# Kernel optimization log

Measured on AMD Instinct MI355X. Metric: run time of the kernel, lower is better.

Reference implementation:

```python
import jax, jax.numpy as jnp
import numpy as np

B, L, C, H = 8, 16384, 128, 4
EPS = 1e-5


def setup_inputs() -> dict:
    key = jax.random.key(0)
    k1, k2, k3, k4 = jax.random.split(key, 4)
    return {
        "x": jax.random.normal(k1, (B, L, C), dtype=jnp.float32),
        "W_qkv": jax.random.normal(k2, (3 * C, C), dtype=jnp.float32) * (C ** -0.5),
        "W_out": jax.random.normal(k3, (C, C), dtype=jnp.float32) * (C ** -0.5),
        "b_out": jax.random.normal(k4, (C,), dtype=jnp.float32) * 0.01,
        "gn_w": jnp.ones((C,), dtype=jnp.float32),
        "gn_b": jnp.zeros((C,), dtype=jnp.float32),
    }


def reference(x, W_qkv, W_out, b_out, gn_w, gn_b):
    b, l, c = x.shape
    h = H
    d = c // h                      # dim_head
    scale = d ** -0.5
    xc = jnp.swapaxes(x, 1, 2)      # [b, c, l]
    # 1x1 conv == channel matmul
    qkv = jnp.einsum('oc,bcl->bol', W_qkv, xc)     # [b, 3c, l]
    q, k, v = jnp.split(qkv, 3, axis=1)
    q = q.reshape(b, h, d, l)
    k = k.reshape(b, h, d, l)
    v = v.reshape(b, h, d, l)
    q = jax.nn.softmax(q, axis=2) * scale          # softmax over head-dim
    k = jax.nn.softmax(k, axis=3)                  # softmax over length
    context = jnp.einsum('bhcj,bhdj->bhcd', k, v)  # [b, h, d, d]
    out = jnp.einsum('bhcd,bhdi->bhci', context, q)  # [b, h, d, l]
    out = out.reshape(b, h * d, l)
    out = jnp.einsum('oc,bcl->bol', W_out, out) + b_out[None, :, None]
    # GroupNorm(1, c): normalize over (channel, length) per sample
    mean = jnp.mean(out, axis=(1, 2), keepdims=True)
    var = jnp.var(out, axis=(1, 2), keepdims=True)
    out = (out - mean) * jax.lax.rsqrt(var + EPS)
    out = out * gn_w[None, :, None] + gn_b[None, :, None]
    return jnp.swapaxes(out, 1, 2)                 # [b, l, c]
```

## Files before the change

### kernel.cpp

```cpp
#include <hip/hip_runtime.h>

#define BATCH 8
#define SEQL 16384
#define NCH 128
#define NH 4
#define HD 32
#define GEPS 1e-5f

typedef __bf16 bf16x8 __attribute__((ext_vector_type(8)));
typedef __bf16 bf16x4 __attribute__((ext_vector_type(4)));
typedef float f32x4 __attribute__((ext_vector_type(4)));

#define WKV_B   0
#define WQ_B    65536
#define WO_B    98304
#define CTXB_B  131072
#define GNS_B   196608
#define CTXP_B  262144


__global__ void k_prep(const float* __restrict__ wqkv, const float* __restrict__ wout,
                       char* __restrict__ wsb) {
    int i = blockIdx.x * 256 + threadIdx.x;
    __bf16* wkvb = (__bf16*)(wsb + WKV_B);
    __bf16* wqb  = (__bf16*)(wsb + WQ_B);
    __bf16* wob  = (__bf16*)(wsb + WO_B);
    if (i < 384 * 128) {
        int o = i >> 7, c = i & 127;
        __bf16 v = (__bf16)wqkv[i];
        if (o < 128) wqb[o * 128 + c] = v;
        else         wkvb[(o - 128) * 128 + c] = v;
    }
    if (i < 128 * 128) wob[i] = (__bf16)wout[i];
    if (i < 16) ((float*)(wsb + GNS_B))[i] = 0.f;
}

__global__ __launch_bounds__(256, 3) void k_pass1(const float* __restrict__ x,
                                                  char* __restrict__ wsb, int P) {
    __shared__ __attribute__((aligned(16))) __bf16 xb[8352];
    __shared__ __attribute__((aligned(16))) __bf16 ekv[16464];
    const int t = threadIdx.x;
    const int lane = t & 63, wave = t >> 6;
    const int n16 = lane & 15, q = lane >> 4;
    const int batch = blockIdx.x / P, sub = blockIdx.x % P;
    const int nrep = 256 / P;
    const __bf16* __restrict__ wkvb = (const __bf16*)(wsb + WKV_B);

    bf16x8 aw[4][4];
#pragma unroll
    for (int mt = 0; mt < 4; mt++)
#pragma unroll
        for (int ks = 0; ks < 4; ks++)
            aw[mt][ks] = *(const bf16x8*)&wkvb[(wave * 64 + mt * 16 + n16) * 128 + ks * 32 + q * 8];

    f32x4 ctxacc[2][2];
#pragma unroll
    for (int i = 0; i < 2; i++)
#pragma unroll
        for (int j = 0; j < 2; j++) ctxacc[i][j] = (f32x4){0.f, 0.f, 0.f, 0.f};
    float zacc[4][4];
#pragma unroll
    for (int i = 0; i < 4; i++)
#pragma unroll
        for (int j = 0; j < 4; j++) zacc[i][j] = 0.f;

    for (int rep = 0; rep < nrep; rep++) {
        const int chunk = sub + rep * P;
        const float* xg = x + (size_t)(batch * SEQL + chunk * 64) * NCH;
#pragma unroll
        for (int r = 0; r < 8; r++) {
            int e = t + r * 256;
            int tok = e >> 5, c4 = (e & 31) * 4;
            float4 v = ((const float4*)xg)[e];
            bf16x4 h; h.x = (__bf16)v.x; h.y = (__bf16)v.y; h.z = (__bf16)v.z; h.w = (__bf16)v.w;
            *(bf16x4*)&xb[(c4 >> 5) * 2088 + ((c4 >> 3) & 3) * 520 + tok * 8 + (c4 & 7)] = h;
        }
        __syncthreads();

#pragma unroll
        for (int half = 0; half < 2; half++) {
            f32x4 kvacc[4][2];
#pragma unroll
            for (int i = 0; i < 4; i++)
#pragma unroll
                for (int j = 0; j < 2; j++) kvacc[i][j] = (f32x4){0.f, 0.f, 0.f, 0.f};
#pragma unroll
            for (int ks = 0; ks < 4; ks++) {
                bf16x8 b[2];
#pragma unroll
                for (int nl = 0; nl < 2; nl++)
                    b[nl] = *(const bf16x8*)&xb[ks * 2088 + q * 520 + ((half * 2 + nl) * 16 + n16) * 8];
#pragma unroll
                for (int mt = 0; mt < 4; mt++)
#pragma unroll
                    for (int nl = 0; nl < 2; nl++)
                        kvacc[mt][nl] = __builtin_amdgcn_mfma_f32_16x16x32_bf16(
                            aw[mt][ks], b[nl], kvacc[mt][nl], 0, 0, 0);
            }
#pragma unroll
            for (int mt = 0; mt < 4; mt++)
#pragma unroll
                for (int nl = 0; nl < 2; nl++) {
                    int tt = (half * 2 + nl) * 16 + n16;
                    int base = (tt >> 5) * 8232 + ((tt >> 3) & 3) * 2056 + (tt & 7);
#pragma unroll
                    for (int r = 0; r < 4; r++) {
                        float vv = kvacc[mt][nl][r];
                        if (wave < 2) { vv = __expf(vv); zacc[mt][r] += vv; }
                        int o = wave * 64 + mt * 16 + q * 4 + r;
                        ekv[base + o * 8] = (__bf16)vv;
                    }
                }
        }
        __syncthreads();

#pragma unroll
        for (int ks2 = 0; ks2 < 2; ks2++) {
            bf16x8 ea[2], vb[2];
#pragma unroll
            for (int ml = 0; ml < 2; ml++) {
                ea[ml] = *(const bf16x8*)&ekv[ks2 * 8232 + q * 2056 + (wave * 32 + ml * 16 + n16) * 8];
                vb[ml] = *(const bf16x8*)&ekv[ks2 * 8232 + q * 2056 + (128 + wave * 32 + ml * 16 + n16) * 8];
            }
#pragma unroll
            for (int ml = 0; ml < 2; ml++)
#pragma unroll
                for (int nl = 0; nl < 2; nl++)
                    ctxacc[ml][nl] = __builtin_amdgcn_mfma_f32_16x16x32_bf16(
                        ea[ml], vb[nl], ctxacc[ml][nl], 0, 0, 0);
        }
        __syncthreads();
    }

    float* ctxp = (float*)(wsb + CTXP_B) + (size_t)blockIdx.x * 4096 + wave * 1024;
#pragma unroll
    for (int ml = 0; ml < 2; ml++)
#pragma unroll
        for (int nl = 0; nl < 2; nl++)
#pragma unroll
            for (int r = 0; r < 4; r++)
                ctxp[(ml * 16 + q * 4 + r) * 32 + nl * 16 + n16] = ctxacc[ml][nl][r];
    if (wave < 2) {
        float* zpT = (float*)(wsb + CTXP_B) + (size_t)BATCH * P * 4096;
#pragma unroll
        for (int mt = 0; mt < 4; mt++)
#pragma unroll
            for (int r = 0; r < 4; r++) {
                float z = zacc[mt][r];
                z += __shfl_xor(z, 1); z += __shfl_xor(z, 2);
                z += __shfl_xor(z, 4); z += __shfl_xor(z, 8);
                if (n16 == 0)
                    zpT[((size_t)batch * 128 + wave * 64 + mt * 16 + q * 4 + r) * P + sub] = z;
            }
    }
}

__global__ __launch_bounds__(256) void k_reduce(char* __restrict__ wsb, int P) {
    __shared__ float red[4][64];
    __shared__ float zw[4];
    const int tid = threadIdx.x;
    const int b = blockIdx.x >> 6, eg = blockIdx.x & 63;
    const int elemBase = eg * 64;
    const float* ctxp = (const float*)(wsb + CTXP_B);
    const float* zpT = ctxp + (size_t)BATCH * P * 4096;

    {
        int hc2 = tid >> 7, pslot = tid & 127;
        float zs = 0.f;
        for (int p = pslot; p < P; p += 128)
            zs += zpT[((size_t)b * 128 + eg * 2 + hc2) * P + p];
#pragma unroll
        for (int off = 32; off > 0; off >>= 1) zs += __shfl_xor(zs, off);
        if ((tid & 63) == 0) zw[tid >> 6] = zs;
    }
    {
        int pg = tid >> 6, e = tid & 63;
        int cnt = P >> 2;
        const float* base = ctxp + ((size_t)(b * P + pg * cnt)) * 4096 + elemBase + e;
        float cs = 0.f;
        for (int k = 0; k < cnt; k++) cs += base[(size_t)k * 4096];
        red[pg][e] = cs;
    }
    __syncthreads();
    if (tid < 64) {
        float tot = red[0][tid] + red[1][tid] + red[2][tid] + red[3][tid];
        float zs = zw[(tid >> 5) * 2] + zw[(tid >> 5) * 2 + 1];
        ((__bf16*)(wsb + CTXB_B))[(size_t)b * 4096 + elemBase + tid] = (__bf16)(tot / zs);
    }
}

__global__ __launch_bounds__(256, 4) void k_pass2(const float* __restrict__ x,
                                                  const float* __restrict__ bout,
                                                  char* __restrict__ wsb,
                                                  float* __restrict__ out) {
    __shared__ __attribute__((aligned(16))) __bf16 xb[8352];
    __shared__ __attribute__((aligned(16))) __bf16 pB[8352];
    __shared__ float gred[8];
    const int t = threadIdx.x;
    const int lane = t & 63, wave = t >> 6;
    const int n16 = lane & 15, q = lane >> 4;
    const int batch = blockIdx.x >> 8, chunk = blockIdx.x & 255;
    const __bf16* __restrict__ wqb = (const __bf16*)(wsb + WQ_B);
    const __bf16* __restrict__ wob = (const __bf16*)(wsb + WO_B);
    const __bf16* __restrict__ ctxb = (const __bf16*)(wsb + CTXB_B);

    const size_t tok0 = (size_t)batch * SEQL + chunk * 64;
    const float* xg = x + tok0 * NCH;
#pragma unroll
    for (int r = 0; r < 8; r++) {
        int e = t + r * 256;
        int tok = e >> 5, c4 = (e & 31) * 4;
        float4 v = ((const float4*)xg)[e];
        bf16x4 h; h.x = (__bf16)v.x; h.y = (__bf16)v.y; h.z = (__bf16)v.z; h.w = (__bf16)v.w;
        *(bf16x4*)&xb[(c4 >> 5) * 2088 + ((c4 >> 3) & 3) * 520 + tok * 8 + (c4 & 7)] = h;
    }
    __syncthreads();

    f32x4 qacc[2][4];
#pragma unroll
    for (int i = 0; i < 2; i++)
#pragma unroll
        for (int j = 0; j < 4; j++) qacc[i][j] = (f32x4){0.f, 0.f, 0.f, 0.f};
#pragma unroll
    for (int ks = 0; ks < 4; ks++) {
        bf16x8 aq_k[2];
#pragma unroll
        for (int ml = 0; ml < 2; ml++)
            aq_k[ml] = *(const bf16x8*)&wqb[(wave * 32 + ml * 16 + n16) * 128 + ks * 32 + q * 8];
        bf16x8 b[4];
#pragma unroll
        for (int nt = 0; nt < 4; nt++)
            b[nt] = *(const bf16x8*)&xb[ks * 2088 + q * 520 + (nt * 16 + n16) * 8];
#pragma unroll
        for (int ml = 0; ml < 2; ml++)
#pragma unroll
            for (int nt = 0; nt < 4; nt++)
                qacc[ml][nt] = __builtin_amdgcn_mfma_f32_16x16x32_bf16(
                    aq_k[ml], b[nt], qacc[ml][nt], 0, 0, 0);
    }
#pragma unroll
    for (int nt = 0; nt < 4; nt++) {
        float ss = 0.f;
#pragma unroll
        for (int ml = 0; ml < 2; ml++)
#pragma unroll
            for (int r = 0; r < 4; r++) {
                float e = __expf(qacc[ml][nt][r]);
                qacc[ml][nt][r] = e;
                ss += e;
            }
        ss += __shfl_xor(ss, 16);
        ss += __shfl_xor(ss, 32);
        float inv = 0.17677669529663687f / ss;
#pragma unroll
        for (int ml = 0; ml < 2; ml++)
#pragma unroll
            for (int r = 0; r < 4; r++) qacc[ml][nt][r] *= inv;
    }
#pragma unroll
    for (int ml = 0; ml < 2; ml++)
#pragma unroll
        for (int nt = 0; nt < 4; nt++) {
            bf16x4 h;
            h.x = (__bf16)qacc[ml][nt][0]; h.y = (__bf16)qacc[ml][nt][1];
            h.z = (__bf16)qacc[ml][nt][2]; h.w = (__bf16)qacc[ml][nt][3];
            *(bf16x4*)&pB[wave * 2088 + (ml * 2 + (q >> 1)) * 520 +
                          (nt * 16 + n16) * 8 + (q & 1) * 4] = h;
        }
    __syncthreads();
    bf16x8 actx[2];
#pragma unroll
    for (int ml = 0; ml < 2; ml++)
        actx[ml] = *(const bf16x8*)&ctxb[((size_t)(batch * 4 + wave) * 32 + ml * 16 + n16) * 32 + q * 8];
    f32x4 aacc[2][4];
#pragma unroll
    for (int ml = 0; ml < 2; ml++)
#pragma unroll
        for (int nt = 0; nt < 4; nt++) {
            bf16x8 pb = *(const bf16x8*)&pB[wave * 2088 + q * 520 + (nt * 16 + n16) * 8];
            aacc[ml][nt] = __builtin_amdgcn_mfma_f32_16x16x32_bf16(
                actx[ml], pb, (f32x4){0.f, 0.f, 0.f, 0.f}, 0, 0, 0);
        }
    __bf16* attB = xb;
#pragma unroll
    for (int ml = 0; ml < 2; ml++)
#pragma unroll
        for (int nt = 0; nt < 4; nt++) {
            bf16x4 h;
            h.x = (__bf16)aacc[ml][nt][0]; h.y = (__bf16)aacc[ml][nt][1];
            h.z = (__bf16)aacc[ml][nt][2]; h.w = (__bf16)aacc[ml][nt][3];
            *(bf16x4*)&attB[wave * 2088 + (ml * 2 + (q >> 1)) * 520 +
                            (nt * 16 + n16) * 8 + (q & 1) * 4] = h;
        }
    __syncthreads();
    f32x4 oacc[2][4];
#pragma unroll
    for (int i = 0; i < 2; i++)
#pragma unroll
        for (int j = 0; j < 4; j++) oacc[i][j] = (f32x4){0.f, 0.f, 0.f, 0.f};
#pragma unroll
    for (int ks = 0; ks < 4; ks++) {
        bf16x8 ao_k[2];
#pragma unroll
        for (int ml = 0; ml < 2; ml++)
            ao_k[ml] = *(const bf16x8*)&wob[(wave * 32 + ml * 16 + n16) * 128 + ks * 32 + q * 8];
        bf16x8 b[4];
#pragma unroll
        for (int nt = 0; nt < 4; nt++)
            b[nt] = *(const bf16x8*)&attB[ks * 2088 + q * 520 + (nt * 16 + n16) * 8];
#pragma unroll
        for (int ml = 0; ml < 2; ml++)
#pragma unroll
            for (int nt = 0; nt < 4; nt++)
                oacc[ml][nt] = __builtin_amdgcn_mfma_f32_16x16x32_bf16(
                    ao_k[ml], b[nt], oacc[ml][nt], 0, 0, 0);
    }
    float4 bias[2];
#pragma unroll
    for (int ml = 0; ml < 2; ml++)
        bias[ml] = *(const float4*)&bout[wave * 32 + ml * 16 + q * 4];
    float s1 = 0.f, s2 = 0.f;
#pragma unroll
    for (int ml = 0; ml < 2; ml++)
#pragma unroll
        for (int nt = 0; nt < 4; nt++) {
            float4 vv;
            vv.x = oacc[ml][nt][0] + bias[ml].x;
            vv.y = oacc[ml][nt][1] + bias[ml].y;
            vv.z = oacc[ml][nt][2] + bias[ml].z;
            vv.w = oacc[ml][nt][3] + bias[ml].w;
            s1 += vv.x + vv.y + vv.z + vv.w;
            s2 += vv.x * vv.x + vv.y * vv.y + vv.z * vv.z + vv.w * vv.w;
            *(float4*)&out[(tok0 + nt * 16 + n16) * NCH + wave * 32 + ml * 16 + q * 4] = vv;
        }
#pragma unroll
    for (int off = 32; off > 0; off >>= 1) {
        s1 += __shfl_xor(s1, off);
        s2 += __shfl_xor(s2, off);
    }
    if (lane == 0) { gred[wave * 2 + 0] = s1; gred[wave * 2 + 1] = s2; }
    __syncthreads();
    if (t < 2) {
        float s = gred[t] + gred[2 + t] + gred[4 + t] + gred[6 + t];
        atomicAdd(&((float*)(wsb + GNS_B))[batch * 2 + t], s);
    }
}

__global__ __launch_bounds__(256) void k_gnorm(float* __restrict__ out,
                                               const char* __restrict__ wsb,
                                               const float* __restrict__ gw,
                                               const float* __restrict__ gb) {
    size_t base4 = ((size_t)blockIdx.x * 256 + threadIdx.x) * 2;
    int b = (int)(base4 >> 19);
    const float* gns = (const float*)(wsb + GNS_B);
    const float n = (float)NCH * (float)SEQL;
    float mean = gns[b * 2] / n;
    float var = gns[b * 2 + 1] / n - mean * mean;
    float rstd = rsqrtf(var + GEPS);
    int cbase = (int)((base4 & 31) * 4);
    float4 w0 = *(const float4*)&gw[cbase];
    float4 w1 = *(const float4*)&gw[cbase + 4];
    float4 b0 = *(const float4*)&gb[cbase];
    float4 b1 = *(const float4*)&gb[cbase + 4];
    float4 v0 = ((float4*)out)[base4];
    float4 v1 = ((float4*)out)[base4 + 1];
    v0.x = (v0.x - mean) * rstd * w0.x + b0.x;
    v0.y = (v0.y - mean) * rstd * w0.y + b0.y;
    v0.z = (v0.z - mean) * rstd * w0.z + b0.z;
    v0.w = (v0.w - mean) * rstd * w0.w + b0.w;
    v1.x = (v1.x - mean) * rstd * w1.x + b1.x;
    v1.y = (v1.y - mean) * rstd * w1.y + b1.y;
    v1.z = (v1.z - mean) * rstd * w1.z + b1.z;
    v1.w = (v1.w - mean) * rstd * w1.w + b1.w;
    ((float4*)out)[base4] = v0;
    ((float4*)out)[base4 + 1] = v1;
}

extern "C" void kernel_launch(void* const* d_in, const int* in_sizes, int n_in,
                              void* d_out, int out_size, void* d_ws, size_t ws_size,
                              hipStream_t stream) {
    const float* x    = (const float*)d_in[0];
    const float* wqkv = (const float*)d_in[1];
    const float* wout = (const float*)d_in[2];
    const float* bout = (const float*)d_in[3];
    const float* gw   = (const float*)d_in[4];
    const float* gb   = (const float*)d_in[5];
    float* out = (float*)d_out;
    char* wsb  = (char*)d_ws;

    int P = 256;
    while (P > 4 &&
           (size_t)CTXP_B + (size_t)BATCH * P * (16384 + 512) > ws_size)
        P >>= 1;

    k_prep<<<192, 256, 0, stream>>>(wqkv, wout, wsb);
    k_pass1<<<BATCH * P, 256, 0, stream>>>(x, wsb, P);
    k_reduce<<<BATCH * 64, 256, 0, stream>>>(wsb, P);
    k_pass2<<<2048, 256, 0, stream>>>(x, bout, wsb, out);
    k_gnorm<<<8192, 256, 0, stream>>>(out, wsb, gw, gb);
}
```

Baseline: 253.1 us.

## Software-pipeline x loads in pass1/pass2 and halve block counts

In pass1, the next chunk of x is now loaded into registers while the current chunk's context MFMAs run, which removes one barrier per iteration. Pass2 now processes two chunks per block and prefetches the second chunk's x the same way, so the grid drops to 1024 blocks. P goes from 256 to 128, which halves the partial-context buffers the reduce kernel has to sum. The partial-context stores become float4 writes with a transposed layout, and k_reduce is reworked to read per-row z sums and write the context transposed to match. In exchange, register pressure rises from the prefetch buffers and there is less parallelism per kernel.

```diff
diff --git a/kernel.cpp b/kernel.cpp
--- a/kernel.cpp
+++ b/kernel.cpp
@@ -64,9 +64,8 @@
 #pragma unroll
         for (int j = 0; j < 4; j++) zacc[i][j] = 0.f;
 
-    for (int rep = 0; rep < nrep; rep++) {
-        const int chunk = sub + rep * P;
-        const float* xg = x + (size_t)(batch * SEQL + chunk * 64) * NCH;
+    {
+        const float* xg = x + (size_t)(batch * SEQL + sub * 64) * NCH;
 #pragma unroll
         for (int r = 0; r < 8; r++) {
             int e = t + r * 256;
@@ -75,8 +74,10 @@
             bf16x4 h; h.x = (__bf16)v.x; h.y = (__bf16)v.y; h.z = (__bf16)v.z; h.w = (__bf16)v.w;
             *(bf16x4*)&xb[(c4 >> 5) * 2088 + ((c4 >> 3) & 3) * 520 + tok * 8 + (c4 & 7)] = h;
         }
+    }
+
+    for (int rep = 0; rep < nrep; rep++) {
         __syncthreads();
-
 #pragma unroll
         for (int half = 0; half < 2; half++) {
             f32x4 kvacc[4][2];
@@ -112,8 +113,14 @@
                     }
                 }
         }
+        float4 vpre[8];
+        const bool hasNext = (rep + 1 < nrep);
+        if (hasNext) {
+            const float* xg2 = x + (size_t)(batch * SEQL + (sub + (rep + 1) * P) * 64) * NCH;
+#pragma unroll
+            for (int r = 0; r < 8; r++) vpre[r] = ((const float4*)xg2)[t + r * 256];
+        }
         __syncthreads();
-
 #pragma unroll
         for (int ks2 = 0; ks2 < 2; ks2++) {
             bf16x8 ea[2], vb[2];
@@ -129,17 +136,29 @@
                     ctxacc[ml][nl] = __builtin_amdgcn_mfma_f32_16x16x32_bf16(
                         ea[ml], vb[nl], ctxacc[ml][nl], 0, 0, 0);
         }
-        __syncthreads();
+        if (hasNext) {
+#pragma unroll
+            for (int r = 0; r < 8; r++) {
+                int e = t + r * 256;
+                int tok = e >> 5, c4 = (e & 31) * 4;
+                bf16x4 h;
+                h.x = (__bf16)vpre[r].x; h.y = (__bf16)vpre[r].y;
+                h.z = (__bf16)vpre[r].z; h.w = (__bf16)vpre[r].w;
+                *(bf16x4*)&xb[(c4 >> 5) * 2088 + ((c4 >> 3) & 3) * 520 + tok * 8 + (c4 & 7)] = h;
+            }
+        }
     }
 
     float* ctxp = (float*)(wsb + CTXP_B) + (size_t)blockIdx.x * 4096 + wave * 1024;
 #pragma unroll
-    for (int ml = 0; ml < 2; ml++)
-#pragma unroll
-        for (int nl = 0; nl < 2; nl++)
-#pragma unroll
-            for (int r = 0; r < 4; r++)
-                ctxp[(ml * 16 + q * 4 + r) * 32 + nl * 16 + n16] = ctxacc[ml][nl][r];
+    for (int nl = 0; nl < 2; nl++)
+#pragma unroll
+        for (int ml = 0; ml < 2; ml++) {
+            float4 v4;
+            v4.x = ctxacc[ml][nl][0]; v4.y = ctxacc[ml][nl][1];
+            v4.z = ctxacc[ml][nl][2]; v4.w = ctxacc[ml][nl][3];
+            *(float4*)&ctxp[(nl * 16 + n16) * 32 + ml * 16 + q * 4] = v4;
+        }
     if (wave < 2) {
         float* zpT = (float*)(wsb + CTXP_B) + (size_t)BATCH * P * 4096;
 #pragma unroll
@@ -157,26 +176,24 @@
 
 __global__ __launch_bounds__(256) void k_reduce(char* __restrict__ wsb, int P) {
     __shared__ float red[4][64];
-    __shared__ float zw[4];
+    __shared__ float zw[32];
     const int tid = threadIdx.x;
     const int b = blockIdx.x >> 6, eg = blockIdx.x & 63;
-    const int elemBase = eg * 64;
     const float* ctxp = (const float*)(wsb + CTXP_B);
     const float* zpT = ctxp + (size_t)BATCH * P * 4096;
 
     {
-        int hc2 = tid >> 7, pslot = tid & 127;
+        int ci = tid >> 3, pslot = tid & 7;
+        size_t row = ((size_t)b * 128 + (size_t)(eg >> 4) * 32 + ci) * P;
         float zs = 0.f;
-        for (int p = pslot; p < P; p += 128)
-            zs += zpT[((size_t)b * 128 + eg * 2 + hc2) * P + p];
-#pragma unroll
-        for (int off = 32; off > 0; off >>= 1) zs += __shfl_xor(zs, off);
-        if ((tid & 63) == 0) zw[tid >> 6] = zs;
+        for (int p = pslot; p < P; p += 8) zs += zpT[row + p];
+        zs += __shfl_xor(zs, 1); zs += __shfl_xor(zs, 2); zs += __shfl_xor(zs, 4);
+        if (pslot == 0) zw[ci] = zs;
     }
     {
         int pg = tid >> 6, e = tid & 63;
         int cnt = P >> 2;
-        const float* base = ctxp + ((size_t)(b * P + pg * cnt)) * 4096 + elemBase + e;
+        const float* base = ctxp + ((size_t)(b * P + pg * cnt)) * 4096 + eg * 64 + e;
         float cs = 0.f;
         for (int k = 0; k < cnt; k++) cs += base[(size_t)k * 4096];
         red[pg][e] = cs;
@@ -184,8 +201,10 @@
     __syncthreads();
     if (tid < 64) {
         float tot = red[0][tid] + red[1][tid] + red[2][tid] + red[3][tid];
-        float zs = zw[(tid >> 5) * 2] + zw[(tid >> 5) * 2 + 1];
-        ((__bf16*)(wsb + CTXB_B))[(size_t)b * 4096 + elemBase + tid] = (__bf16)(tot / zs);
+        int e = eg * 64 + tid;
+        int h = e >> 10, d = (e >> 5) & 31, c = e & 31;
+        ((__bf16*)(wsb + CTXB_B))[((size_t)b << 12) + (h << 10) + (c << 5) + d] =
+            (__bf16)(tot / zw[c]);
     }
 }
 
@@ -199,140 +218,173 @@
     const int t = threadIdx.x;
     const int lane = t & 63, wave = t >> 6;
     const int n16 = lane & 15, q = lane >> 4;
-    const int batch = blockIdx.x >> 8, chunk = blockIdx.x & 255;
+    const int batch = blockIdx.x >> 7, sub = blockIdx.x & 127;
     const __bf16* __restrict__ wqb = (const __bf16*)(wsb + WQ_B);
     const __bf16* __restrict__ wob = (const __bf16*)(wsb + WO_B);
     const __bf16* __restrict__ ctxb = (const __bf16*)(wsb + CTXB_B);
 
-    const size_t tok0 = (size_t)batch * SEQL + chunk * 64;
-    const float* xg = x + tok0 * NCH;
-#pragma unroll
-    for (int r = 0; r < 8; r++) {
-        int e = t + r * 256;
-        int tok = e >> 5, c4 = (e & 31) * 4;
-        float4 v = ((const float4*)xg)[e];
-        bf16x4 h; h.x = (__bf16)v.x; h.y = (__bf16)v.y; h.z = (__bf16)v.z; h.w = (__bf16)v.w;
-        *(bf16x4*)&xb[(c4 >> 5) * 2088 + ((c4 >> 3) & 3) * 520 + tok * 8 + (c4 & 7)] = h;
-    }
-    __syncthreads();
-
-    f32x4 qacc[2][4];
-#pragma unroll
-    for (int i = 0; i < 2; i++)
-#pragma unroll
-        for (int j = 0; j < 4; j++) qacc[i][j] = (f32x4){0.f, 0.f, 0.f, 0.f};
-#pragma unroll
-    for (int ks = 0; ks < 4; ks++) {
-        bf16x8 aq_k[2];
-#pragma unroll
-        for (int ml = 0; ml < 2; ml++)
-            aq_k[ml] = *(const bf16x8*)&wqb[(wave * 32 + ml * 16 + n16) * 128 + ks * 32 + q * 8];
-        bf16x8 b[4];
-#pragma unroll
-        for (int nt = 0; nt < 4; nt++)
-            b[nt] = *(const bf16x8*)&xb[ks * 2088 + q * 520 + (nt * 16 + n16) * 8];
-#pragma unroll
-        for (int ml = 0; ml < 2; ml++)
-#pragma unroll
-            for (int nt = 0; nt < 4; nt++)
-                qacc[ml][nt] = __builtin_amdgcn_mfma_f32_16x16x32_bf16(
-                    aq_k[ml], b[nt], qacc[ml][nt], 0, 0, 0);
-    }
-#pragma unroll
-    for (int nt = 0; nt < 4; nt++) {
-        float ss = 0.f;
-#pragma unroll
-        for (int ml = 0; ml < 2; ml++)
-#pragma unroll
-            for (int r = 0; r < 4; r++) {
-                float e = __expf(qacc[ml][nt][r]);
-                qacc[ml][nt][r] = e;
-                ss += e;
-            }
-        ss += __shfl_xor(ss, 16);
-        ss += __shfl_xor(ss, 32);
-        float inv = 0.17677669529663687f / ss;
-#pragma unroll
-        for (int ml = 0; ml < 2; ml++)
-#pragma unroll
-            for (int r = 0; r < 4; r++) qacc[ml][nt][r] *= inv;
-    }
-#pragma unroll
-    for (int ml = 0; ml < 2; ml++)
-#pragma unroll
-        for (int nt = 0; nt < 4; nt++) {
-            bf16x4 h;
-            h.x = (__bf16)qacc[ml][nt][0]; h.y = (__bf16)qacc[ml][nt][1];
-            h.z = (__bf16)qacc[ml][nt][2]; h.w = (__bf16)qacc[ml][nt][3];
-            *(bf16x4*)&pB[wave * 2088 + (ml * 2 + (q >> 1)) * 520 +
-                          (nt * 16 + n16) * 8 + (q & 1) * 4] = h;
-        }
-    __syncthreads();
     bf16x8 actx[2];
 #pragma unroll
     for (int ml = 0; ml < 2; ml++)
         actx[ml] = *(const bf16x8*)&ctxb[((size_t)(batch * 4 + wave) * 32 + ml * 16 + n16) * 32 + q * 8];
-    f32x4 aacc[2][4];
-#pragma unroll
-    for (int ml = 0; ml < 2; ml++)
-#pragma unroll
-        for (int nt = 0; nt < 4; nt++) {
-            bf16x8 pb = *(const bf16x8*)&pB[wave * 2088 + q * 520 + (nt * 16 + n16) * 8];
-            aacc[ml][nt] = __builtin_amdgcn_mfma_f32_16x16x32_bf16(
-                actx[ml], pb, (f32x4){0.f, 0.f, 0.f, 0.f}, 0, 0, 0);
-        }
-    __bf16* attB = xb;
-#pragma unroll
-    for (int ml = 0; ml < 2; ml++)
-#pragma unroll
-        for (int nt = 0; nt < 4; nt++) {
-            bf16x4 h;
-            h.x = (__bf16)aacc[ml][nt][0]; h.y = (__bf16)aacc[ml][nt][1];
-            h.z = (__bf16)aacc[ml][nt][2]; h.w = (__bf16)aacc[ml][nt][3];
-            *(bf16x4*)&attB[wave * 2088 + (ml * 2 + (q >> 1)) * 520 +
-                            (nt * 16 + n16) * 8 + (q & 1) * 4] = h;
-        }
-    __syncthreads();
-    f32x4 oacc[2][4];
-#pragma unroll
-    for (int i = 0; i < 2; i++)
-#pragma unroll
-        for (int j = 0; j < 4; j++) oacc[i][j] = (f32x4){0.f, 0.f, 0.f, 0.f};
-#pragma unroll
-    for (int ks = 0; ks < 4; ks++) {
-        bf16x8 ao_k[2];
-#pragma unroll
-        for (int ml = 0; ml < 2; ml++)
-            ao_k[ml] = *(const bf16x8*)&wob[(wave * 32 + ml * 16 + n16) * 128 + ks * 32 + q * 8];
-        bf16x8 b[4];
-#pragma unroll
-        for (int nt = 0; nt < 4; nt++)
-            b[nt] = *(const bf16x8*)&attB[ks * 2088 + q * 520 + (nt * 16 + n16) * 8];
-#pragma unroll
-        for (int ml = 0; ml < 2; ml++)
-#pragma unroll
-            for (int nt = 0; nt < 4; nt++)
-                oacc[ml][nt] = __builtin_amdgcn_mfma_f32_16x16x32_bf16(
-                    ao_k[ml], b[nt], oacc[ml][nt], 0, 0, 0);
-    }
     float4 bias[2];
 #pragma unroll
     for (int ml = 0; ml < 2; ml++)
         bias[ml] = *(const float4*)&bout[wave * 32 + ml * 16 + q * 4];
+
+    {
+        const float* xg = x + (size_t)(batch * SEQL + sub * 64) * NCH;
+#pragma unroll
+        for (int r = 0; r < 8; r++) {
+            int e = t + r * 256;
+            int tok = e >> 5, c4 = (e & 31) * 4;
+            float4 v = ((const float4*)xg)[e];
+            bf16x4 h; h.x = (__bf16)v.x; h.y = (__bf16)v.y; h.z = (__bf16)v.z; h.w = (__bf16)v.w;
+            *(bf16x4*)&xb[(c4 >> 5) * 2088 + ((c4 >> 3) & 3) * 520 + tok * 8 + (c4 & 7)] = h;
+        }
+    }
+
     float s1 = 0.f, s2 = 0.f;
-#pragma unroll
-    for (int ml = 0; ml < 2; ml++)
+    bf16x4 hpre[8];
+
+#pragma unroll
+    for (int rep = 0; rep < 2; rep++) {
+        const int chunk = sub + rep * 128;
+        const size_t tok0 = (size_t)batch * SEQL + chunk * 64;
+        __syncthreads();
+        f32x4 qacc[2][4];
+#pragma unroll
+        for (int i = 0; i < 2; i++)
+#pragma unroll
+            for (int j = 0; j < 4; j++) qacc[i][j] = (f32x4){0.f, 0.f, 0.f, 0.f};
+#pragma unroll
+        for (int ks = 0; ks < 4; ks++) {
+            bf16x8 aq_k[2];
+#pragma unroll
+            for (int ml = 0; ml < 2; ml++)
+                aq_k[ml] = *(const bf16x8*)&wqb[(wave * 32 + ml * 16 + n16) * 128 + ks * 32 + q * 8];
+            bf16x8 b[4];
+#pragma unroll
+            for (int nt = 0; nt < 4; nt++)
+                b[nt] = *(const bf16x8*)&xb[ks * 2088 + q * 520 + (nt * 16 + n16) * 8];
+#pragma unroll
+            for (int ml = 0; ml < 2; ml++)
+#pragma unroll
+                for (int nt = 0; nt < 4; nt++)
+                    qacc[ml][nt] = __builtin_amdgcn_mfma_f32_16x16x32_bf16(
+                        aq_k[ml], b[nt], qacc[ml][nt], 0, 0, 0);
+        }
+        float4 vpre[8];
+        if (rep == 0) {
+            const float* xg2 = x + (size_t)(batch * SEQL + (sub + 128) * 64) * NCH;
+#pragma unroll
+            for (int r = 0; r < 8; r++) vpre[r] = ((const float4*)xg2)[t + r * 256];
+        }
 #pragma unroll
         for (int nt = 0; nt < 4; nt++) {
-            float4 vv;
-            vv.x = oacc[ml][nt][0] + bias[ml].x;
-            vv.y = oacc[ml][nt][1] + bias[ml].y;
-            vv.z = oacc[ml][nt][2] + bias[ml].z;
-            vv.w = oacc[ml][nt][3] + bias[ml].w;
-            s1 += vv.x + vv.y + vv.z + vv.w;
-            s2 += vv.x * vv.x + vv.y * vv.y + vv.z * vv.z + vv.w * vv.w;
-            *(float4*)&out[(tok0 + nt * 16 + n16) * NCH + wave * 32 + ml * 16 + q * 4] = vv;
-        }
+            float ss = 0.f;
+#pragma unroll
+            for (int ml = 0; ml < 2; ml++)
+#pragma unroll
+                for (int r = 0; r < 4; r++) {
+                    float e = __expf(qacc[ml][nt][r]);
+                    qacc[ml][nt][r] = e;
+                    ss += e;
+                }
+            ss += __shfl_xor(ss, 16);
+            ss += __shfl_xor(ss, 32);
+            float inv = 0.17677669529663687f / ss;
+#pragma unroll
+            for (int ml = 0; ml < 2; ml++)
+#pragma unroll
+                for (int r = 0; r < 4; r++) qacc[ml][nt][r] *= inv;
+        }
+#pragma unroll
+        for (int ml = 0; ml < 2; ml++)
+#pragma unroll
+            for (int nt = 0; nt < 4; nt++) {
+                bf16x4 h;
+                h.x = (__bf16)qacc[ml][nt][0]; h.y = (__bf16)qacc[ml][nt][1];
+                h.z = (__bf16)qacc[ml][nt][2]; h.w = (__bf16)qacc[ml][nt][3];
+                *(bf16x4*)&pB[wave * 2088 + (ml * 2 + (q >> 1)) * 520 +
+                              (nt * 16 + n16) * 8 + (q & 1) * 4] = h;
+            }
+        __syncthreads();
+        f32x4 aacc[2][4];
+#pragma unroll
+        for (int ml = 0; ml < 2; ml++)
+#pragma unroll
+            for (int nt = 0; nt < 4; nt++) {
+                bf16x8 pb = *(const bf16x8*)&pB[wave * 2088 + q * 520 + (nt * 16 + n16) * 8];
+                aacc[ml][nt] = __builtin_amdgcn_mfma_f32_16x16x32_bf16(
+                    actx[ml], pb, (f32x4){0.f, 0.f, 0.f, 0.f}, 0, 0, 0);
+            }
+        if (rep == 0) {
+#pragma unroll
+            for (int r = 0; r < 8; r++) {
+                bf16x4 h;
+                h.x = (__bf16)vpre[r].x; h.y = (__bf16)vpre[r].y;
+                h.z = (__bf16)vpre[r].z; h.w = (__bf16)vpre[r].w;
+                hpre[r] = h;
+            }
+        }
+        __bf16* attB = xb;
+#pragma unroll
+        for (int ml = 0; ml < 2; ml++)
+#pragma unroll
+            for (int nt = 0; nt < 4; nt++) {
+                bf16x4 h;
+                h.x = (__bf16)aacc[ml][nt][0]; h.y = (__bf16)aacc[ml][nt][1];
+                h.z = (__bf16)aacc[ml][nt][2]; h.w = (__bf16)aacc[ml][nt][3];
+                *(bf16x4*)&attB[wave * 2088 + (ml * 2 + (q >> 1)) * 520 +
+                                (nt * 16 + n16) * 8 + (q & 1) * 4] = h;
+            }
+        __syncthreads();
+        f32x4 oacc[2][4];
+#pragma unroll
+        for (int i = 0; i < 2; i++)
+#pragma unroll
+            for (int j = 0; j < 4; j++) oacc[i][j] = (f32x4){0.f, 0.f, 0.f, 0.f};
+#pragma unroll
+        for (int ks = 0; ks < 4; ks++) {
+            bf16x8 ao_k[2];
+#pragma unroll
+            for (int ml = 0; ml < 2; ml++)
+                ao_k[ml] = *(const bf16x8*)&wob[(wave * 32 + ml * 16 + n16) * 128 + ks * 32 + q * 8];
+            bf16x8 b[4];
+#pragma unroll
+            for (int nt = 0; nt < 4; nt++)
+                b[nt] = *(const bf16x8*)&attB[ks * 2088 + q * 520 + (nt * 16 + n16) * 8];
+#pragma unroll
+            for (int ml = 0; ml < 2; ml++)
+#pragma unroll
+                for (int nt = 0; nt < 4; nt++)
+                    oacc[ml][nt] = __builtin_amdgcn_mfma_f32_16x16x32_bf16(
+                        ao_k[ml], b[nt], oacc[ml][nt], 0, 0, 0);
+        }
+#pragma unroll
+        for (int ml = 0; ml < 2; ml++)
+#pragma unroll
+            for (int nt = 0; nt < 4; nt++) {
+                float4 vv;
+                vv.x = oacc[ml][nt][0] + bias[ml].x;
+                vv.y = oacc[ml][nt][1] + bias[ml].y;
+                vv.z = oacc[ml][nt][2] + bias[ml].z;
+                vv.w = oacc[ml][nt][3] + bias[ml].w;
+                s1 += vv.x + vv.y + vv.z + vv.w;
+                s2 += vv.x * vv.x + vv.y * vv.y + vv.z * vv.z + vv.w * vv.w;
+                *(float4*)&out[(tok0 + nt * 16 + n16) * NCH + wave * 32 + ml * 16 + q * 4] = vv;
+            }
+        if (rep == 0) {
+            __syncthreads();
+#pragma unroll
+            for (int r = 0; r < 8; r++) {
+                int e = t + r * 256;
+                int tok = e >> 5, c4 = (e & 31) * 4;
+                *(bf16x4*)&xb[(c4 >> 5) * 2088 + ((c4 >> 3) & 3) * 520 + tok * 8 + (c4 & 7)] = hpre[r];
+            }
+        }
+    }
 #pragma unroll
     for (int off = 32; off > 0; off >>= 1) {
         s1 += __shfl_xor(s1, off);
@@ -388,7 +440,7 @@
     float* out = (float*)d_out;
     char* wsb  = (char*)d_ws;
 
-    int P = 256;
+    int P = 128;
     while (P > 4 &&
            (size_t)CTXP_B + (size_t)BATCH * P * (16384 + 512) > ws_size)
         P >>= 1;
@@ -396,6 +448,6 @@
     k_prep<<<192, 256, 0, stream>>>(wqkv, wout, wsb);
     k_pass1<<<BATCH * P, 256, 0, stream>>>(x, wsb, P);
     k_reduce<<<BATCH * 64, 256, 0, stream>>>(wsb, P);
-    k_pass2<<<2048, 256, 0, stream>>>(x, bout, wsb, out);
+    k_pass2<<<1024, 256, 0, stream>>>(x, bout, wsb, out);
     k_gnorm<<<8192, 256, 0, stream>>>(out, wsb, gw, gb);
 }
```

After: 261.9 us. 1.03x slower.
